# Kernel optimization log

Hardware: AMD Instinct MI355X
Metric: run time of the kernel (lower is better)

The kernel has to match this reference:

```python
import jax, jax.numpy as jnp
import numpy as np

B, N, K, F, H = 4, 1024, 100, 42, 64


def setup_inputs() -> dict:
    key = jax.random.key(0)
    ks = jax.random.split(key, 10)
    return {
        "image": jax.random.normal(ks[0], (B, N, F), jnp.float32),
        "dfeat": jax.random.normal(ks[1], (B, N, K, F, 3), jnp.float32) * 0.1,
        "neighbor": jax.random.randint(ks[2], (B, N, K), 0, N + 1, jnp.int32),
        "Egroup_weight": jax.random.uniform(ks[3], (B, N, N), jnp.float32),
        "divider": jnp.ones((B, N), jnp.float32),
        # fitting-net params (single atom type), cfg [F, H, H, 1], tanh
        "W1": jax.random.normal(ks[4], (F, H), jnp.float32) * 0.1,
        "b1": jnp.zeros((H,), jnp.float32),
        "W2": jax.random.normal(ks[5], (H, H), jnp.float32) * 0.1,
        "b2": jnp.zeros((H,), jnp.float32),
        "W3": jax.random.normal(ks[6], (H, 1), jnp.float32) * 0.1,
        "b3": jnp.zeros((1,), jnp.float32),
    }


def reference(image, dfeat, neighbor, Egroup_weight, divider, W1, b1, W2, b2, W3, b3):
    b, n, f = image.shape
    k = neighbor.shape[-1]

    def energy(x):  # per-atom energy: [..., F] -> [...]
        h = jnp.tanh(x @ W1 + b1)
        h = jnp.tanh(h @ W2 + b2)
        return (h @ W3 + b3)[..., 0]

    Ei = energy(image)                                   # [B, N]
    # dEi/dFeat: each Ei depends only on its own feature row, so grad of sum
    # gives the per-atom Jacobian rows (the autograd=True f_FC path).
    dE = jax.grad(lambda x: energy(x).sum())(image)      # [B, N, F]
    Etot = jnp.sum(Ei, axis=1)                           # [B]

    # Fortran 1-based neighbor indices; row 0 of the padded table is zeros
    # (neighbor==0 means "no neighbor").
    dE_pad = jnp.concatenate([jnp.zeros((b, 1, f), dE.dtype), dE], axis=1)  # [B, N+1, F]
    flat = dE_pad.reshape(b * (n + 1), f)
    offs = jnp.repeat(jnp.arange(b, dtype=jnp.int32) * (n + 1), n * k)
    idx = neighbor.reshape(-1).astype(jnp.int32) + offs
    dEi_nb = flat[idx].reshape(b, n, k, f)               # gather   [B, N, K, F]
    # Force[b,i,:] = sum_j dE[neighbor(i,j)] . dfeat[b,i,j]  (reduce over K, F)
    Force = jnp.einsum('bnkf,bnkfd->bnd', dEi_nb, dfeat)  # [B, N, 3]
    return Etot, Ei, Force
```

## Files before the change

kernel.cpp:

```cpp
#include <hip/hip_runtime.h>

#define B 4
#define N 1024
#define K 100
#define F 42
#define H 64

__global__ __launch_bounds__(256) void mlp_kernel(
    const float* __restrict__ image,
    const float* __restrict__ W1, const float* __restrict__ b1,
    const float* __restrict__ W2, const float* __restrict__ b2,
    const float* __restrict__ W3, const float* __restrict__ b3,
    float* __restrict__ Ei, float* __restrict__ dE)
{
    __shared__ float W1s[F][H + 1];
    __shared__ float W2s[H][H + 1];
    __shared__ float xsh[4][F];
    __shared__ float h1sh[4][H];
    __shared__ float aux[4][H];

    const int tid  = threadIdx.x;
    const int lane = tid & 63;
    const int wave = tid >> 6;
    const int atom = blockIdx.x * 4 + wave;

    for (int idx = tid; idx < F * H; idx += 256)
        W1s[idx >> 6][idx & 63] = W1[idx];
    for (int idx = tid; idx < H * H; idx += 256)
        W2s[idx >> 6][idx & 63] = W2[idx];
    if (lane < F) xsh[wave][lane] = image[atom * F + lane];
    __syncthreads();

    float a1 = b1[lane];
    #pragma unroll
    for (int f = 0; f < F; ++f) a1 = fmaf(xsh[wave][f], W1s[f][lane], a1);
    const float h1 = tanhf(a1);
    h1sh[wave][lane] = h1;
    __syncthreads();

    float a2 = b2[lane];
    #pragma unroll 8
    for (int j = 0; j < H; ++j) a2 = fmaf(h1sh[wave][j], W2s[j][lane], a2);
    const float h2 = tanhf(a2);
    const float w3 = W3[lane];

    float t = h2 * w3;
    #pragma unroll
    for (int off = 32; off > 0; off >>= 1) t += __shfl_down(t, off);
    if (lane == 0) Ei[atom] = t + b3[0];

    aux[wave][lane] = w3 * (1.0f - h2 * h2);
    __syncthreads();

    float s = 0.0f;
    #pragma unroll 8
    for (int j = 0; j < H; ++j) s = fmaf(W2s[lane][j], aux[wave][j], s);
    const float g1 = s * (1.0f - h1 * h1);
    h1sh[wave][lane] = g1;
    __syncthreads();

    if (lane < F) {
        float dx = 0.0f;
        #pragma unroll 8
        for (int i = 0; i < H; ++i) dx = fmaf(W1s[lane][i], h1sh[wave][i], dx);
        dE[atom * F + lane] = dx;
    }
}

__global__ __launch_bounds__(256) void force_kernel(
    const float* __restrict__ dE, const float* __restrict__ dfeat,
    const int* __restrict__ neighbor, const float* __restrict__ Ei,
    float* __restrict__ force, float* __restrict__ Etot)
{
    __shared__ int   nsh[K];
    __shared__ float red[4][3];

    const int tid  = threadIdx.x;
    const int bid  = blockIdx.x;
    const int lane = tid & 63, wave = tid >> 6;

    if (bid >= B * N) {
        const int b = bid - B * N;
        float s = 0.0f;
        for (int i = tid; i < N; i += 256) s += Ei[b * N + i];
        #pragma unroll
        for (int off = 32; off > 0; off >>= 1) s += __shfl_down(s, off);
        if (lane == 0) red[wave][0] = s;
        __syncthreads();
        if (tid == 0)
            Etot[b] = (red[0][0] + red[1][0]) + (red[2][0] + red[3][0]);
        return;
    }

    const int bn = bid;
    const int b  = bn >> 10;

    if (tid < K) nsh[tid] = neighbor[bn * K + tid];
    __syncthreads();

    const float* df  = dfeat + (size_t)bn * (K * F * 3);
    const float* dEb = dE + (size_t)b * (N * F);

    float fx = 0.0f, fy = 0.0f, fz = 0.0f;
    for (int p = tid; p < K * F; p += 256) {
        const int k  = p / F;
        const int f  = p - k * F;
        const int nb = nsh[k];
        const float de = (nb > 0) ? dEb[(nb - 1) * F + f] : 0.0f;
        const int base = p * 3;
        fx = fmaf(de, df[base + 0], fx);
        fy = fmaf(de, df[base + 1], fy);
        fz = fmaf(de, df[base + 2], fz);
    }

    #pragma unroll
    for (int off = 32; off > 0; off >>= 1) {
        fx += __shfl_down(fx, off);
        fy += __shfl_down(fy, off);
        fz += __shfl_down(fz, off);
    }
    if (lane == 0) { red[wave][0] = fx; red[wave][1] = fy; red[wave][2] = fz; }
    __syncthreads();
    if (tid == 0) {
        force[bn * 3 + 0] = (red[0][0] + red[1][0]) + (red[2][0] + red[3][0]);
        force[bn * 3 + 1] = (red[0][1] + red[1][1]) + (red[2][1] + red[3][1]);
        force[bn * 3 + 2] = (red[0][2] + red[1][2]) + (red[2][2] + red[3][2]);
    }
}

extern "C" void kernel_launch(void* const* d_in, const int* in_sizes, int n_in,
                              void* d_out, int out_size, void* d_ws, size_t ws_size,
                              hipStream_t stream)
{
    const float* image    = (const float*)d_in[0];
    const float* dfeat    = (const float*)d_in[1];
    const int*   neighbor = (const int*)d_in[2];
    const float* W1 = (const float*)d_in[5];
    const float* b1 = (const float*)d_in[6];
    const float* W2 = (const float*)d_in[7];
    const float* b2 = (const float*)d_in[8];
    const float* W3 = (const float*)d_in[9];
    const float* b3 = (const float*)d_in[10];

    float* out   = (float*)d_out;
    float* Etot  = out;
    float* Ei    = out + B;
    float* Force = out + B + B * N;
    float* dE    = (float*)d_ws;

    mlp_kernel<<<(B * N) / 4, 256, 0, stream>>>(image, W1, b1, W2, b2, W3, b3, Ei, dE);
    force_kernel<<<B * N + B, 256, 0, stream>>>(dE, dfeat, neighbor, Ei, Force, Etot);
}
```

Baseline: 50.18 us.

## Restructure MLP kernel so each lane owns an atom and waves split hidden units

The MLP kernel now processes 64 atoms per 512-thread block. Each lane holds one atom's features in registers, and each wave computes a slice of hidden units. Weights are read as wave-uniform global loads instead of being staged per block in shared memory, and the forward and backward activations are exchanged through shared memory. This is meant to cut the repeated per-block weight loading and the low per-wave ALU use of the old one-atom-per-wave layout. The cost is higher register pressure and far fewer blocks (64 instead of 1024), which may leave the GPU underoccupied.

```diff
diff --git a/kernel.cpp b/kernel.cpp
--- a/kernel.cpp
+++ b/kernel.cpp
@@ -6,64 +6,137 @@
 #define F 42
 #define H 64
 
-__global__ __launch_bounds__(256) void mlp_kernel(
+#define APB 64
+#define NW  8
+#define IPW (H / NW)
+
+__global__ __launch_bounds__(512) void mlp_kernel(
     const float* __restrict__ image,
     const float* __restrict__ W1, const float* __restrict__ b1,
     const float* __restrict__ W2, const float* __restrict__ b2,
     const float* __restrict__ W3, const float* __restrict__ b3,
     float* __restrict__ Ei, float* __restrict__ dE)
 {
-    __shared__ float W1s[F][H + 1];
-    __shared__ float W2s[H][H + 1];
-    __shared__ float xsh[4][F];
-    __shared__ float h1sh[4][H];
-    __shared__ float aux[4][H];
+    __shared__ float xsh[APB][F + 1];
+    __shared__ float h1sh[H][APB];
+    __shared__ float g2sh[H][APB];
+    __shared__ float g1sh[H][APB];
+    __shared__ float esh[NW][APB];
+    __shared__ float dsh[APB][F + 1];
 
     const int tid  = threadIdx.x;
     const int lane = tid & 63;
-    const int wave = tid >> 6;
-    const int atom = blockIdx.x * 4 + wave;
-
-    for (int idx = tid; idx < F * H; idx += 256)
-        W1s[idx >> 6][idx & 63] = W1[idx];
-    for (int idx = tid; idx < H * H; idx += 256)
-        W2s[idx >> 6][idx & 63] = W2[idx];
-    if (lane < F) xsh[wave][lane] = image[atom * F + lane];
-    __syncthreads();
-
-    float a1 = b1[lane];
-    #pragma unroll
-    for (int f = 0; f < F; ++f) a1 = fmaf(xsh[wave][f], W1s[f][lane], a1);
-    const float h1 = tanhf(a1);
-    h1sh[wave][lane] = h1;
-    __syncthreads();
-
-    float a2 = b2[lane];
-    #pragma unroll 8
-    for (int j = 0; j < H; ++j) a2 = fmaf(h1sh[wave][j], W2s[j][lane], a2);
-    const float h2 = tanhf(a2);
-    const float w3 = W3[lane];
-
-    float t = h2 * w3;
-    #pragma unroll
-    for (int off = 32; off > 0; off >>= 1) t += __shfl_down(t, off);
-    if (lane == 0) Ei[atom] = t + b3[0];
-
-    aux[wave][lane] = w3 * (1.0f - h2 * h2);
-    __syncthreads();
-
-    float s = 0.0f;
-    #pragma unroll 8
-    for (int j = 0; j < H; ++j) s = fmaf(W2s[lane][j], aux[wave][j], s);
-    const float g1 = s * (1.0f - h1 * h1);
-    h1sh[wave][lane] = g1;
-    __syncthreads();
-
-    if (lane < F) {
-        float dx = 0.0f;
-        #pragma unroll 8
-        for (int i = 0; i < H; ++i) dx = fmaf(W1s[lane][i], h1sh[wave][i], dx);
-        dE[atom * F + lane] = dx;
+    const int w    = tid >> 6;
+    const int a0   = blockIdx.x * APB;
+    const int i0   = w * IPW;
+
+    for (int idx = tid; idx < APB * F; idx += 512) {
+        const int a = idx / F, f = idx - a * F;
+        xsh[a][f] = image[(size_t)a0 * F + idx];
+    }
+    __syncthreads();
+
+    float x[F];
+    #pragma unroll
+    for (int f = 0; f < F; ++f) x[f] = xsh[lane][f];
+
+    float acc[IPW];
+    #pragma unroll
+    for (int ii = 0; ii < IPW; ++ii) acc[ii] = b1[i0 + ii];
+    #pragma unroll 6
+    for (int f = 0; f < F; ++f) {
+        #pragma unroll
+        for (int ii = 0; ii < IPW; ++ii)
+            acc[ii] = fmaf(x[f], W1[f * H + i0 + ii], acc[ii]);
+    }
+    float h1l[IPW];
+    #pragma unroll
+    for (int ii = 0; ii < IPW; ++ii) {
+        h1l[ii] = tanhf(acc[ii]);
+        h1sh[i0 + ii][lane] = h1l[ii];
+    }
+    __syncthreads();
+
+    #pragma unroll
+    for (int ii = 0; ii < IPW; ++ii) acc[ii] = b2[i0 + ii];
+    #pragma unroll
+    for (int jc = 0; jc < H / 16; ++jc) {
+        float hv[16];
+        #pragma unroll
+        for (int t = 0; t < 16; ++t) hv[t] = h1sh[jc * 16 + t][lane];
+        #pragma unroll
+        for (int t = 0; t < 16; ++t)
+            #pragma unroll
+            for (int ii = 0; ii < IPW; ++ii)
+                acc[ii] = fmaf(hv[t], W2[(jc * 16 + t) * H + i0 + ii], acc[ii]);
+    }
+
+    float ep = 0.0f;
+    #pragma unroll
+    for (int ii = 0; ii < IPW; ++ii) {
+        const float h2 = tanhf(acc[ii]);
+        const float w3 = W3[i0 + ii];
+        ep = fmaf(h2, w3, ep);
+        g2sh[i0 + ii][lane] = w3 * (1.0f - h2 * h2);
+    }
+    esh[w][lane] = ep;
+    __syncthreads();
+
+    if (w == 0) {
+        float e = b3[0];
+        #pragma unroll
+        for (int q = 0; q < NW; ++q) e += esh[q][lane];
+        Ei[a0 + lane] = e;
+    }
+
+    float s[IPW];
+    #pragma unroll
+    for (int jj = 0; jj < IPW; ++jj) s[jj] = 0.0f;
+    #pragma unroll
+    for (int ic = 0; ic < H / 16; ++ic) {
+        float gv[16];
+        #pragma unroll
+        for (int t = 0; t < 16; ++t) gv[t] = g2sh[ic * 16 + t][lane];
+        #pragma unroll
+        for (int jj = 0; jj < IPW; ++jj)
+            #pragma unroll
+            for (int t = 0; t < 16; ++t)
+                s[jj] = fmaf(gv[t], W2[(i0 + jj) * H + ic * 16 + t], s[jj]);
+    }
+    #pragma unroll
+    for (int jj = 0; jj < IPW; ++jj)
+        g1sh[i0 + jj][lane] = s[jj] * (1.0f - h1l[jj] * h1l[jj]);
+    __syncthreads();
+
+    {
+        const int fbase = (w < 4) ? (w * 6) : (24 + (w - 4) * 5);
+        const int nf    = (w < 4) ? 6 : ((w < 7) ? 5 : 3);
+        float s2[6];
+        #pragma unroll
+        for (int q = 0; q < 6; ++q) s2[q] = 0.0f;
+        #pragma unroll
+        for (int jc = 0; jc < H / 16; ++jc) {
+            float gv[16];
+            #pragma unroll
+            for (int t = 0; t < 16; ++t) gv[t] = g1sh[jc * 16 + t][lane];
+            #pragma unroll
+            for (int q = 0; q < 6; ++q) {
+                if (q < nf) {
+                    #pragma unroll
+                    for (int t = 0; t < 16; ++t)
+                        s2[q] = fmaf(gv[t], W1[(fbase + q) * H + jc * 16 + t], s2[q]);
+                }
+            }
+        }
+        #pragma unroll
+        for (int q = 0; q < 6; ++q)
+            if (q < nf) dsh[lane][fbase + q] = s2[q];
+    }
+    __syncthreads();
+
+    for (int idx = tid; idx < APB * F; idx += 512) {
+        const int a = idx / F, f = idx - a * F;
+        dE[(size_t)a0 * F + idx] = dsh[a][f];
     }
 }
 
@@ -148,6 +221,6 @@
     float* Force = out + B + B * N;
     float* dE    = (float*)d_ws;
 
-    mlp_kernel<<<(B * N) / 4, 256, 0, stream>>>(image, W1, b1, W2, b2, W3, b3, Ei, dE);
+    mlp_kernel<<<(B * N) / APB, 512, 0, stream>>>(image, W1, b1, W2, b2, W3, b3, Ei, dE);
     force_kernel<<<B * N + B, 256, 0, stream>>>(dE, dfeat, neighbor, Ei, Force, Etot);
 }
```

Measured after the change: 181.2 us. +261.1%, slower.

## Process four atoms per wave in MLP kernel with vectorized LDS reads

Applied to the files above, without the earlier changes.

Each wave now evaluates the forward and backward MLP for four atoms instead of one, so each block covers 16 atoms. This reuses every weight value loaded from LDS across four atoms and cuts how often the weight matrices are copied into LDS. Inner products use 128-bit LDS loads over padded rows, and block-wide syncs after staging are replaced by wave barriers. The cost is more registers per thread and fewer blocks, while the dominant force kernel is unchanged.

```diff
diff --git a/kernel.cpp b/kernel.cpp
--- a/kernel.cpp
+++ b/kernel.cpp
@@ -5,6 +5,14 @@
 #define K 100
 #define F 42
 #define H 64
+
+#define APW 4
+#define NWV 4
+#define APB (APW * NWV)
+#define PW  68
+#define PX  44
+
+typedef float f32x4 __attribute__((ext_vector_type(4)));
 
 __global__ __launch_bounds__(256) void mlp_kernel(
     const float* __restrict__ image,
@@ -13,57 +21,122 @@
     const float* __restrict__ W3, const float* __restrict__ b3,
     float* __restrict__ Ei, float* __restrict__ dE)
 {
-    __shared__ float W1s[F][H + 1];
-    __shared__ float W2s[H][H + 1];
-    __shared__ float xsh[4][F];
-    __shared__ float h1sh[4][H];
-    __shared__ float aux[4][H];
+    __shared__ __align__(16) float W1s[F][PW];
+    __shared__ __align__(16) float W2s[H][PW];
+    __shared__ __align__(16) float xsh[APB][PX];
+    __shared__ __align__(16) float h1sh[NWV][APW][H];
+    __shared__ __align__(16) float g2sh[NWV][APW][H];
+    __shared__ __align__(16) float g1sh[NWV][APW][H];
 
     const int tid  = threadIdx.x;
     const int lane = tid & 63;
-    const int wave = tid >> 6;
-    const int atom = blockIdx.x * 4 + wave;
+    const int wv   = tid >> 6;
+    const int a0   = blockIdx.x * APB;
+    const int aw   = a0 + wv * APW;
 
     for (int idx = tid; idx < F * H; idx += 256)
         W1s[idx >> 6][idx & 63] = W1[idx];
     for (int idx = tid; idx < H * H; idx += 256)
         W2s[idx >> 6][idx & 63] = W2[idx];
-    if (lane < F) xsh[wave][lane] = image[atom * F + lane];
+    for (int idx = tid; idx < APB * F; idx += 256) {
+        const int a = idx / F, f = idx - a * F;
+        xsh[a][f] = image[(size_t)a0 * F + idx];
+    }
     __syncthreads();
 
-    float a1 = b1[lane];
-    #pragma unroll
-    for (int f = 0; f < F; ++f) a1 = fmaf(xsh[wave][f], W1s[f][lane], a1);
-    const float h1 = tanhf(a1);
-    h1sh[wave][lane] = h1;
-    __syncthreads();
-
-    float a2 = b2[lane];
-    #pragma unroll 8
-    for (int j = 0; j < H; ++j) a2 = fmaf(h1sh[wave][j], W2s[j][lane], a2);
-    const float h2 = tanhf(a2);
+    float acc[APW];
+    {
+        const float bb = b1[lane];
+        #pragma unroll
+        for (int a = 0; a < APW; ++a) acc[a] = bb;
+    }
+    #pragma unroll
+    for (int fc = 0; fc < 10; ++fc) {
+        float wv4[4];
+        #pragma unroll
+        for (int t = 0; t < 4; ++t) wv4[t] = W1s[4 * fc + t][lane];
+        #pragma unroll
+        for (int a = 0; a < APW; ++a) {
+            const f32x4 xv = *(const f32x4*)&xsh[wv * APW + a][4 * fc];
+            #pragma unroll
+            for (int t = 0; t < 4; ++t) acc[a] = fmaf(xv[t], wv4[t], acc[a]);
+        }
+    }
+    #pragma unroll
+    for (int f = 40; f < F; ++f) {
+        const float w = W1s[f][lane];
+        #pragma unroll
+        for (int a = 0; a < APW; ++a) acc[a] = fmaf(xsh[wv * APW + a][f], w, acc[a]);
+    }
+    float h1l[APW];
+    #pragma unroll
+    for (int a = 0; a < APW; ++a) {
+        h1l[a] = tanhf(acc[a]);
+        h1sh[wv][a][lane] = h1l[a];
+    }
+    __builtin_amdgcn_wave_barrier();
+
+    {
+        const float bb = b2[lane];
+        #pragma unroll
+        for (int a = 0; a < APW; ++a) acc[a] = bb;
+    }
+    #pragma unroll
+    for (int jc = 0; jc < H / 4; ++jc) {
+        float wv4[4];
+        #pragma unroll
+        for (int t = 0; t < 4; ++t) wv4[t] = W2s[4 * jc + t][lane];
+        #pragma unroll
+        for (int a = 0; a < APW; ++a) {
+            const f32x4 hv = *(const f32x4*)&h1sh[wv][a][4 * jc];
+            #pragma unroll
+            for (int t = 0; t < 4; ++t) acc[a] = fmaf(hv[t], wv4[t], acc[a]);
+        }
+    }
     const float w3 = W3[lane];
-
-    float t = h2 * w3;
-    #pragma unroll
-    for (int off = 32; off > 0; off >>= 1) t += __shfl_down(t, off);
-    if (lane == 0) Ei[atom] = t + b3[0];
-
-    aux[wave][lane] = w3 * (1.0f - h2 * h2);
-    __syncthreads();
-
-    float s = 0.0f;
-    #pragma unroll 8
-    for (int j = 0; j < H; ++j) s = fmaf(W2s[lane][j], aux[wave][j], s);
-    const float g1 = s * (1.0f - h1 * h1);
-    h1sh[wave][lane] = g1;
-    __syncthreads();
+    const float bias3 = b3[0];
+    #pragma unroll
+    for (int a = 0; a < APW; ++a) {
+        const float h2 = tanhf(acc[a]);
+        g2sh[wv][a][lane] = w3 * (1.0f - h2 * h2);
+        float t = h2 * w3;
+        #pragma unroll
+        for (int off = 32; off > 0; off >>= 1) t += __shfl_down(t, off);
+        if (lane == 0) Ei[aw + a] = t + bias3;
+    }
+    __builtin_amdgcn_wave_barrier();
+
+    float s[APW] = {0.f, 0.f, 0.f, 0.f};
+    #pragma unroll
+    for (int ic = 0; ic < H / 4; ++ic) {
+        const f32x4 wr = *(const f32x4*)&W2s[lane][4 * ic];
+        #pragma unroll
+        for (int a = 0; a < APW; ++a) {
+            const f32x4 gv = *(const f32x4*)&g2sh[wv][a][4 * ic];
+            #pragma unroll
+            for (int t = 0; t < 4; ++t) s[a] = fmaf(wr[t], gv[t], s[a]);
+        }
+    }
+    #pragma unroll
+    for (int a = 0; a < APW; ++a)
+        g1sh[wv][a][lane] = s[a] * (1.0f - h1l[a] * h1l[a]);
+    __builtin_amdgcn_wave_barrier();
 
     if (lane < F) {
-        float dx = 0.0f;
-        #pragma unroll 8
-        for (int i = 0; i < H; ++i) dx = fmaf(W1s[lane][i], h1sh[wave][i], dx);
-        dE[atom * F + lane] = dx;
+        float dx[APW] = {0.f, 0.f, 0.f, 0.f};
+        #pragma unroll
+        for (int ic = 0; ic < H / 4; ++ic) {
+            const f32x4 wr = *(const f32x4*)&W1s[lane][4 * ic];
+            #pragma unroll
+            for (int a = 0; a < APW; ++a) {
+                const f32x4 gv = *(const f32x4*)&g1sh[wv][a][4 * ic];
+                #pragma unroll
+                for (int t = 0; t < 4; ++t) dx[a] = fmaf(wr[t], gv[t], dx[a]);
+            }
+        }
+        #pragma unroll
+        for (int a = 0; a < APW; ++a)
+            dE[(size_t)(aw + a) * F + lane] = dx[a];
     }
 }
 
@@ -148,6 +221,6 @@
     float* Force = out + B + B * N;
     float* dE    = (float*)d_ws;
 
-    mlp_kernel<<<(B * N) / 4, 256, 0, stream>>>(image, W1, b1, W2, b2, W3, b3, Ei, dE);
+    mlp_kernel<<<(B * N) / APB, 256, 0, stream>>>(image, W1, b1, W2, b2, W3, b3, Ei, dE);
     force_kernel<<<B * N + B, 256, 0, stream>>>(dE, dfeat, neighbor, Ei, Force, Etot);
 }
```

New measurement: 49.67 us. No clear change (-1.0%).
